# Kernel tuning notes

Hardware: AMD Instinct MI355X
Metric: run time of the kernel (lower is better)

The kernel has to match this reference:

```python
import jax, jax.numpy as jnp
import numpy as np

B, S, M, E, H = 2, 2048, 2048, 1024, 16
D = E // H
LN_EPS = 1e-5


def setup_inputs() -> dict:
    key = jax.random.key(0)
    ks = jax.random.split(key, 14)
    w = lambda k: jax.random.normal(k, (E, E), dtype=jnp.float32) * 0.02
    return {
        "query": jax.random.normal(ks[0], (B, S, E), dtype=jnp.float32),
        "keys": jax.random.normal(ks[1], (B, M, E), dtype=jnp.float32),
        "values": jax.random.normal(ks[2], (B, M, E), dtype=jnp.float32),
        "Wq": w(ks[3]), "bq": jnp.zeros((E,), jnp.float32),
        "Wk": w(ks[4]), "bk": jnp.zeros((E,), jnp.float32),
        "Wv": w(ks[5]), "bv": jnp.zeros((E,), jnp.float32),
        "Wo": w(ks[6]), "bo": jnp.zeros((E,), jnp.float32),
        "gamma": jnp.ones((E,), jnp.float32),
        "beta": jnp.zeros((E,), jnp.float32),
    }


def reference(query, keys, values, Wq, bq, Wk, bk, Wv, bv, Wo, bo, gamma, beta):
    b, s, e = query.shape
    m = keys.shape[1]
    # projections (torch Linear: x @ W.T + b), split heads -> [b, H, len, D]
    Q = (jnp.einsum('bse,fe->bsf', query, Wq) + bq).reshape(b, s, H, D).transpose(0, 2, 1, 3)
    K = (jnp.einsum('bme,fe->bmf', keys, Wk) + bk).reshape(b, m, H, D).transpose(0, 2, 1, 3)
    V = (jnp.einsum('bme,fe->bmf', values, Wv) + bv).reshape(b, m, H, D).transpose(0, 2, 1, 3)
    scores = jnp.einsum('bhsd,bhmd->bhsm', Q, K) / np.sqrt(D).astype(np.float32)
    attn = jax.nn.softmax(scores, axis=-1)  # [b,H,s,m]; dropout is eval no-op
    attended = jnp.einsum('bhsm,bhmd->bhsd', attn, V)
    attended = attended.transpose(0, 2, 1, 3).reshape(b, s, e)
    y = jnp.einsum('bse,fe->bsf', attended, Wo) + bo + query
    mu = jnp.mean(y, axis=-1, keepdims=True)
    var = jnp.mean(jnp.square(y - mu), axis=-1, keepdims=True)
    out = (y - mu) * jax.lax.rsqrt(var + LN_EPS) * gamma + beta
    avg_attention = attn.mean(axis=1)  # [b,s,m]
    return out, avg_attention
```

## Files before the change

kernel.cpp:

```cpp
#include <hip/hip_runtime.h>
#include <hip/hip_bf16.h>

typedef unsigned short u16;
typedef unsigned int   u32;
typedef __attribute__((ext_vector_type(2)))  float fx2;
typedef __attribute__((ext_vector_type(4)))  float fx4;
typedef __attribute__((ext_vector_type(16))) float f32x16;
typedef __attribute__((ext_vector_type(4)))  u16   usx4;
typedef __attribute__((ext_vector_type(8)))  u16   usx8;
typedef __attribute__((ext_vector_type(8)))  __bf16 bf16x8;
typedef __attribute__((ext_vector_type(2)))  int   i32x2;
typedef __attribute__((ext_vector_type(2)))  u32   u32x2;
typedef __attribute__((ext_vector_type(4)))  u32   u32x4;

#define DEVI static __device__ __forceinline__

constexpr int Bb = 2, Ss = 2048, Mm = 2048, Ee = 1024, Hh = 16, Dd = 64;
#define QSCALE 0.18033688011112042f

DEVI u16 f2bf(float f) {
  u32 u = __builtin_bit_cast(u32, f);
  u32 r = (u + 0x7fffu + ((u >> 16) & 1u)) >> 16;
  return (u16)r;
}
DEVI float bf2f(u16 v) {
  u32 u = ((u32)v) << 16;
  return __builtin_bit_cast(float, u);
}
DEVI bf16x8 as_bf(usx8 v) { return __builtin_bit_cast(bf16x8, v); }

DEVI void gld16(const u16* g, u16* l) {
  __builtin_amdgcn_global_load_lds((const __attribute__((address_space(1))) void*)g,
                                   (__attribute__((address_space(3))) void*)l, 16, 0, 0);
}

#if __has_builtin(__builtin_amdgcn_exp2f)
DEVI float xexp2(float x) { return __builtin_amdgcn_exp2f(x); }
#else
DEVI float xexp2(float x) { return exp2f(x); }
#endif

DEVI u32 cvtpk(float lo, float hi) {
  u32 r;
  asm("v_cvt_pk_bf16_f32 %0, %1, %2" : "=v"(r) : "v"(lo), "v"(hi));
  return r;
}
DEVI bf16x8 pa_from(u32 w0, u32 w1, u32 w2, u32 w3) {
  union { u32 u[4]; usx8 v; } t;
  t.u[0] = w0; t.u[1] = w1; t.u[2] = w2; t.u[3] = w3;
  return as_bf(t.v);
}

__global__ __launch_bounds__(256)
void cast_all(const float* __restrict__ q, const float* __restrict__ k,
              const float* __restrict__ v,
              const float* __restrict__ wq, const float* __restrict__ wk,
              const float* __restrict__ wv, const float* __restrict__ wo,
              u16* __restrict__ qc, u16* __restrict__ kc, u16* __restrict__ vc,
              u16* __restrict__ wqc, u16* __restrict__ wkc,
              u16* __restrict__ wvc, u16* __restrict__ woc)
{
  const int y = blockIdx.y;
  const float* s; u16* d; size_t n;
  const size_t NI = (size_t)Bb * Ss * Ee;
  const size_t NW = (size_t)Ee * Ee;
  switch (y) {
    case 0: s = q;  d = qc;  n = NI; break;
    case 1: s = k;  d = kc;  n = NI; break;
    case 2: s = v;  d = vc;  n = NI; break;
    case 3: s = wq; d = wqc; n = NW; break;
    case 4: s = wk; d = wkc; n = NW; break;
    case 5: s = wv; d = wvc; n = NW; break;
    default: s = wo; d = woc; n = NW; break;
  }
  const size_t stride = (size_t)gridDim.x * 256 * 8;
  for (size_t i = ((size_t)blockIdx.x * 256 + threadIdx.x) * 8; i < n; i += stride) {
    fx4 a = *(const fx4*)(s + i);
    fx4 b = *(const fx4*)(s + i + 4);
    u32x4 o;
    o[0] = cvtpk(a[0], a[1]); o[1] = cvtpk(a[2], a[3]);
    o[2] = cvtpk(b[0], b[1]); o[3] = cvtpk(b[2], b[3]);
    *(u32x4*)(d + i) = o;
  }
}

__global__ __launch_bounds__(256, 2)
void gemm_qkv(const u16* __restrict__ qc, const u16* __restrict__ kc,
              const u16* __restrict__ vc,
              const u16* __restrict__ wqc, const u16* __restrict__ wkc,
              const u16* __restrict__ wvc,
              const float* __restrict__ bq, const float* __restrict__ bk,
              const float* __restrict__ bv,
              u16* __restrict__ Qbf, u16* __restrict__ Kbf, u16* __restrict__ Vt)
{
  __shared__ u16 As[2][128][64];
  __shared__ u16 Bs[2][64][64];
  const int tid = threadIdx.x;
  const int w = tid >> 6, l = tid & 63, g = l >> 4, ln = l & 15;
  const int wr = w >> 1, wc = w & 1;

  const int lid = blockIdx.x;
  const int wg = (lid & 7) * 192 + (lid >> 3);
  const int z = wg >> 9;
  const int rem = wg & 511;
  const int row0 = (rem >> 4) * 128;
  const int col0 = (rem & 15) * 64;

  const u16* A = (z == 0) ? qc : (z == 1) ? kc : vc;
  const u16* W = (z == 0) ? wqc : (z == 1) ? wkc : wvc;
  const float* bias = (z == 0) ? bq : (z == 1) ? bk : bv;

  const int colu = (((l & 7) ^ (l >> 3)) << 3);
  auto stage = [&](int buf, int kt) {
#pragma unroll
    for (int j = 0; j < 4; j++) {
      const int c = j * 4 + w;
      const int row = c * 8 + (l >> 3);
      gld16(A + (size_t)(row0 + row) * 1024 + kt * 64 + colu,
            &As[buf][0][0] + c * 512 + l * 8);
    }
#pragma unroll
    for (int j = 0; j < 2; j++) {
      const int c = j * 4 + w;
      const int row = c * 8 + (l >> 3);
      gld16(W + (size_t)(col0 + row) * 1024 + kt * 64 + colu,
            &Bs[buf][0][0] + c * 512 + l * 8);
    }
  };

  fx4 acc[4][2];
#pragma unroll
  for (int i = 0; i < 4; i++)
#pragma unroll
    for (int j = 0; j < 2; j++) acc[i][j] = fx4{0.f, 0.f, 0.f, 0.f};

  stage(0, 0);
  __syncthreads();

  const int swA = (ln & 7) << 3;
  const int NK = 1024 / 64;
  for (int kt = 0; kt < NK; kt++) {
    const int buf = kt & 1;
    if (kt + 1 < NK) stage(buf ^ 1, kt + 1);
#pragma unroll
    for (int ks = 0; ks < 2; ks++) {
      bf16x8 af[4], bfr[2];
      const int cb = (ks * 32 + g * 8) ^ swA;
#pragma unroll
      for (int mi = 0; mi < 4; mi++)
        af[mi] = as_bf(*(const usx8*)&As[buf][wr * 64 + mi * 16 + ln][cb]);
#pragma unroll
      for (int nj = 0; nj < 2; nj++)
        bfr[nj] = as_bf(*(const usx8*)&Bs[buf][wc * 32 + nj * 16 + ln][cb]);
      __builtin_amdgcn_s_setprio(1);
#pragma unroll
      for (int mi = 0; mi < 4; mi++)
#pragma unroll
        for (int nj = 0; nj < 2; nj++)
          acc[mi][nj] = __builtin_amdgcn_mfma_f32_16x16x32_bf16(af[mi], bfr[nj], acc[mi][nj], 0, 0, 0);
      __builtin_amdgcn_s_setprio(0);
    }
    __syncthreads();
  }

#pragma unroll
  for (int mi = 0; mi < 4; mi++) {
#pragma unroll
    for (int nj = 0; nj < 2; nj++) {
      const int j = col0 + wc * 32 + nj * 16 + ln;
      const float bj = bias[j];
      if (z == 2) {
        const int i0 = row0 + wr * 64 + mi * 16 + g * 4;
        const int b2 = i0 >> 11, m2 = i0 & 2047;
        const int h2 = j >> 6,  d2 = j & 63;
        u32x2 pk;
        pk[0] = cvtpk(acc[mi][nj][0] + bj, acc[mi][nj][1] + bj);
        pk[1] = cvtpk(acc[mi][nj][2] + bj, acc[mi][nj][3] + bj);
        *(u32x2*)&Vt[(((size_t)b2 * Hh + h2) * 64 + d2) * (size_t)Mm + m2] = pk;
      } else {
        u16* outp = (z == 0) ? Qbf : Kbf;
        const float sc = (z == 0) ? QSCALE : 1.0f;
#pragma unroll
        for (int r = 0; r < 4; r++) {
          const int i = row0 + wr * 64 + mi * 16 + g * 4 + r;
          outp[(size_t)i * 1024 + j] = f2bf((acc[mi][nj][r] + bj) * sc);
        }
      }
    }
  }
}

__global__ __launch_bounds__(256, 2)
void gemm_out(const u16* __restrict__ Ab, const u16* __restrict__ W,
              const float* __restrict__ bias, const u16* __restrict__ resid,
              u16* __restrict__ outb)
{
  __shared__ u16 As[2][128][64];
  __shared__ u16 Bs[2][64][64];
  const int tid = threadIdx.x;
  const int w = tid >> 6, l = tid & 63, g = l >> 4, ln = l & 15;
  const int wr = w >> 1, wc = w & 1;

  const int lid = blockIdx.x;
  const int wg = (lid & 7) * 64 + (lid >> 3);
  const int row0 = (wg >> 4) * 128;
  const int col0 = (wg & 15) * 64;

  const int colu = (((l & 7) ^ (l >> 3)) << 3);
  auto stage = [&](int buf, int kt) {
#pragma unroll
    for (int j = 0; j < 4; j++) {
      const int c = j * 4 + w;
      const int row = c * 8 + (l >> 3);
      gld16(Ab + (size_t)(row0 + row) * 1024 + kt * 64 + colu,
            &As[buf][0][0] + c * 512 + l * 8);
    }
#pragma unroll
    for (int j = 0; j < 2; j++) {
      const int c = j * 4 + w;
      const int row = c * 8 + (l >> 3);
      gld16(W + (size_t)(col0 + row) * 1024 + kt * 64 + colu,
            &Bs[buf][0][0] + c * 512 + l * 8);
    }
  };

  fx4 acc[4][2];
#pragma unroll
  for (int i = 0; i < 4; i++)
#pragma unroll
    for (int j = 0; j < 2; j++) acc[i][j] = fx4{0.f, 0.f, 0.f, 0.f};

  stage(0, 0);
  __syncthreads();

  const int swA = (ln & 7) << 3;
  const int NK = 1024 / 64;
  for (int kt = 0; kt < NK; kt++) {
    const int buf = kt & 1;
    if (kt + 1 < NK) stage(buf ^ 1, kt + 1);
#pragma unroll
    for (int ks = 0; ks < 2; ks++) {
      bf16x8 af[4], bfr[2];
      const int cb = (ks * 32 + g * 8) ^ swA;
#pragma unroll
      for (int mi = 0; mi < 4; mi++)
        af[mi] = as_bf(*(const usx8*)&As[buf][wr * 64 + mi * 16 + ln][cb]);
#pragma unroll
      for (int nj = 0; nj < 2; nj++)
        bfr[nj] = as_bf(*(const usx8*)&Bs[buf][wc * 32 + nj * 16 + ln][cb]);
      __builtin_amdgcn_s_setprio(1);
#pragma unroll
      for (int mi = 0; mi < 4; mi++)
#pragma unroll
        for (int nj = 0; nj < 2; nj++)
          acc[mi][nj] = __builtin_amdgcn_mfma_f32_16x16x32_bf16(af[mi], bfr[nj], acc[mi][nj], 0, 0, 0);
      __builtin_amdgcn_s_setprio(0);
    }
    __syncthreads();
  }

#pragma unroll
  for (int mi = 0; mi < 4; mi++) {
#pragma unroll
    for (int nj = 0; nj < 2; nj++) {
      const int j = col0 + wc * 32 + nj * 16 + ln;
      const float bj = bias[j];
#pragma unroll
      for (int r = 0; r < 4; r++) {
        const int i = row0 + wr * 64 + mi * 16 + g * 4 + r;
        const float v = acc[mi][nj][r] + bj + bf2f(resid[(size_t)i * 1024 + j]);
        outb[(size_t)i * 1024 + j] = f2bf(v);
      }
    }
  }
}

__global__ __launch_bounds__(256, 2)
void flash_fwd(const u16* __restrict__ Qb, const u16* __restrict__ Kb,
               const u16* __restrict__ Vt, u16* __restrict__ attended,
               float* __restrict__ stats)
{
  __shared__ u16 Ks[2][128][64];
  __shared__ u16 Vs[2][64][128];
  const int tid = threadIdx.x;
  const int w = tid >> 6, l = tid & 63;
  const int ln32 = l & 31, hi = l >> 5;
  const int st = blockIdx.x, h = blockIdx.y, b = blockIdx.z;
  const int s0 = st * 128 + w * 32;

  const u16* Kbase = Kb + (size_t)b * Mm * 1024 + h * 64;
  const u16* Vbase = Vt + ((size_t)(b * Hh + h) * 64) * (size_t)Mm;

  const int colu_k = (((l & 7) ^ (l >> 3)) << 3);
  auto stage = [&](int buf, int mt) {
    const int mb = mt * 128;
#pragma unroll
    for (int j = 0; j < 4; j++) {
      const int c = j * 4 + w;
      const int krow = c * 8 + (l >> 3);
      gld16(Kbase + (size_t)(mb + krow) * 1024 + colu_k,
            &Ks[buf][0][0] + c * 512 + l * 8);
      const int vrow = c * 4 + (l >> 4);
      const int colv = (((l & 15) ^ (vrow & 15)) << 3);
      gld16(Vbase + (size_t)vrow * (size_t)Mm + mb + colv,
            &Vs[buf][0][0] + c * 512 + l * 8);
    }
  };

  bf16x8 qa[4];
#pragma unroll
  for (int dstep = 0; dstep < 4; dstep++)
    qa[dstep] = as_bf(*(const usx8*)(Qb + (size_t)(b * Ss + s0 + ln32) * Ee
                                     + h * 64 + dstep * 16 + hi * 8));

  f32x16 acc[2];
#pragma unroll
  for (int i = 0; i < 16; i++) { acc[0][i] = 0.f; acc[1][i] = 0.f; }
  float lsum = 0.f;

  stage(0, 0);
  __syncthreads();

  const int NT = Mm / 128;
  for (int mt = 0; mt < NT; mt++) {
    const int buf = mt & 1;
    if (mt + 1 < NT) stage(buf ^ 1, mt + 1);

    f32x16 sc[4];
#pragma unroll
    for (int mtile = 0; mtile < 4; mtile++) {
      const int row = mtile * 32 + ln32;
      const int sw = (row & 7) << 3;
      f32x16 c;
#pragma unroll
      for (int i = 0; i < 16; i++) c[i] = 0.f;
#pragma unroll
      for (int dstep = 0; dstep < 4; dstep++) {
        bf16x8 kf = as_bf(*(const usx8*)&Ks[buf][row][(dstep * 16 + hi * 8) ^ sw]);
        c = __builtin_amdgcn_mfma_f32_32x32x16_bf16(kf, qa[dstep], c, 0, 0, 0);
      }
      sc[mtile] = c;
    }

#pragma unroll
    for (int mtile = 0; mtile < 4; mtile++) {
      float p[16];
#pragma unroll
      for (int r = 0; r < 16; r++) p[r] = xexp2(sc[mtile][r]);
      float t0 = (p[0] + p[1]) + (p[2] + p[3]);
      float t1 = (p[4] + p[5]) + (p[6] + p[7]);
      float t2 = (p[8] + p[9]) + (p[10] + p[11]);
      float t3 = (p[12] + p[13]) + (p[14] + p[15]);
      lsum += (t0 + t1) + (t2 + t3);

      u32 cp[8];
#pragma unroll
      for (int i = 0; i < 8; i++) cp[i] = cvtpk(p[2 * i], p[2 * i + 1]);
      i32x2 sA = __builtin_amdgcn_permlane32_swap((int)cp[0], (int)cp[2], false, false);
      i32x2 sB = __builtin_amdgcn_permlane32_swap((int)cp[1], (int)cp[3], false, false);
      bf16x8 pa0 = pa_from((u32)sA.x, (u32)sB.x, (u32)sA.y, (u32)sB.y);
      i32x2 sC = __builtin_amdgcn_permlane32_swap((int)cp[4], (int)cp[6], false, false);
      i32x2 sD = __builtin_amdgcn_permlane32_swap((int)cp[5], (int)cp[7], false, false);
      bf16x8 pa1 = pa_from((u32)sC.x, (u32)sD.x, (u32)sC.y, (u32)sD.y);

#pragma unroll
      for (int dtile = 0; dtile < 2; dtile++) {
        const int vrow = dtile * 32 + ln32;
        const int vsw = (vrow & 15) << 3;
        bf16x8 vb0 = as_bf(*(const usx8*)&Vs[buf][vrow][(mtile * 32 + hi * 8) ^ vsw]);
        bf16x8 vb1 = as_bf(*(const usx8*)&Vs[buf][vrow][(mtile * 32 + 16 + hi * 8) ^ vsw]);
        acc[dtile] = __builtin_amdgcn_mfma_f32_32x32x16_bf16(pa0, vb0, acc[dtile], 0, 0, 0);
        acc[dtile] = __builtin_amdgcn_mfma_f32_32x32x16_bf16(pa1, vb1, acc[dtile], 0, 0, 0);
      }
    }
    __syncthreads();
  }

  lsum += __shfl_xor(lsum, 32);
  const float inv = 1.0f / lsum;
  if (l < 32)
    stats[(size_t)(b * Hh + h) * Ss + s0 + l] = inv;
#pragma unroll
  for (int r = 0; r < 16; r++) {
    const int srow = (r & 3) + 8 * (r >> 2) + 4 * hi;
    const float invr = __shfl(inv, srow);
    const int s_abs = s0 + srow;
#pragma unroll
    for (int dtile = 0; dtile < 2; dtile++)
      attended[(size_t)(b * Ss + s_abs) * Ee + h * 64 + dtile * 32 + ln32] =
          f2bf(acc[dtile][r] * invr);
  }
}

__global__ __launch_bounds__(256)
void avg_attn(const u16* __restrict__ Qb, const u16* __restrict__ Kb,
              const float* __restrict__ stats, float* __restrict__ avg_out)
{
  __shared__ u16 Ks[3][64][64];
  const int tid = threadIdx.x;
  const int w = tid >> 6, l = tid & 63;
  const int ln32 = l & 31, hi = l >> 5;
  const int mtile0 = blockIdx.x, stile = blockIdx.y, b = blockIdx.z;
  const int m0 = mtile0 * 64;
  const int s0 = stile * 128 + w * 32;
  const int s_lane = s0 + ln32;

  const u16* Kbase = Kb + (size_t)(b * Mm + m0) * 1024;
  const u16* Qrow  = Qb + (size_t)(b * Ss + s_lane) * Ee;
  const float* strow = stats + (size_t)b * Hh * Ss + s_lane;

  const int colu = (((l & 7) ^ (l >> 3)) << 3);
  auto stage = [&](int slot, int h) {
#pragma unroll
    for (int j = 0; j < 2; j++) {
      const int c = j * 4 + w;
      const int row = c * 8 + (l >> 3);
      gld16(Kbase + (size_t)row * 1024 + h * 64 + colu,
            &Ks[slot][0][0] + c * 512 + l * 8);
    }
  };

  f32x16 acc[2];
#pragma unroll
  for (int i = 0; i < 16; i++) { acc[0][i] = 0.f; acc[1][i] = 0.f; }

  stage(0, 0);
  stage(1, 1);
  asm volatile("s_waitcnt vmcnt(2)" ::: "memory");
  __builtin_amdgcn_s_barrier();

  for (int h = 0; h < Hh; h++) {
    const int slot = h % 3;

    bf16x8 qa[4];
#pragma unroll
    for (int d = 0; d < 4; d++)
      qa[d] = as_bf(*(const usx8*)(Qrow + h * 64 + d * 16 + hi * 8));
    const float invh = strow[(size_t)h * Ss];

    if (h + 2 < Hh) stage((h + 2) % 3, h + 2);

#pragma unroll
    for (int mtile = 0; mtile < 2; mtile++) {
      const int row = mtile * 32 + ln32;
      const int sw = (row & 7) << 3;
      f32x16 c;
#pragma unroll
      for (int i = 0; i < 16; i++) c[i] = 0.f;
      __builtin_amdgcn_s_setprio(1);
#pragma unroll
      for (int dstep = 0; dstep < 4; dstep++) {
        bf16x8 kf = as_bf(*(const usx8*)&Ks[slot][row][(dstep * 16 + hi * 8) ^ sw]);
        c = __builtin_amdgcn_mfma_f32_32x32x16_bf16(kf, qa[dstep], c, 0, 0, 0);
      }
      __builtin_amdgcn_s_setprio(0);
#pragma unroll
      for (int r = 0; r < 16; r++)
        acc[mtile][r] += xexp2(c[r]) * invh;
    }

    if (h + 2 < Hh) {
      asm volatile("s_waitcnt vmcnt(2)" ::: "memory");
    } else {
      asm volatile("s_waitcnt vmcnt(0)" ::: "memory");
    }
    __builtin_amdgcn_s_barrier();
  }

  float* orow = avg_out + ((size_t)(b * Ss + s_lane)) * Mm + m0;
#pragma unroll
  for (int mtile = 0; mtile < 2; mtile++)
#pragma unroll
    for (int rq = 0; rq < 4; rq++) {
      fx4 o;
#pragma unroll
      for (int j = 0; j < 4; j++) o[j] = acc[mtile][rq * 4 + j] * (1.0f / 16.0f);
      *(fx4*)(orow + mtile * 32 + rq * 8 + 4 * hi) = o;
    }
}

__global__ __launch_bounds__(256)
void ln_kernel(const u16* __restrict__ yb, const float* __restrict__ gamma,
               const float* __restrict__ beta, float* __restrict__ out)
{
  const int row = blockIdx.x, tid = threadIdx.x;
  const int w = tid >> 6, l = tid & 63;
  usx4 v4 = *(const usx4*)(yb + (size_t)row * 1024 + tid * 4);
  float v[4];
#pragma unroll
  for (int j = 0; j < 4; j++) v[j] = bf2f(v4[j]);
  float s = v[0] + v[1] + v[2] + v[3];
  float s2 = v[0] * v[0] + v[1] * v[1] + v[2] * v[2] + v[3] * v[3];
#pragma unroll
  for (int off = 32; off >= 1; off >>= 1) {
    s += __shfl_xor(s, off);
    s2 += __shfl_xor(s2, off);
  }
  __shared__ float rs[4], rq[4];
  if (l == 0) { rs[w] = s; rq[w] = s2; }
  __syncthreads();
  s = (rs[0] + rs[1]) + (rs[2] + rs[3]);
  s2 = (rq[0] + rq[1]) + (rq[2] + rq[3]);
  const float mu = s * (1.0f / 1024.0f);
  const float var = s2 * (1.0f / 1024.0f) - mu * mu;
  const float rstd = rsqrtf(var + 1e-5f);
  fx4 gm = *(const fx4*)(gamma + tid * 4);
  fx4 bt = *(const fx4*)(beta + tid * 4);
  fx4 o;
#pragma unroll
  for (int j = 0; j < 4; j++) o[j] = (v[j] - mu) * rstd * gm[j] + bt[j];
  *(fx4*)(out + (size_t)row * 1024 + tid * 4) = o;
}

extern "C" void kernel_launch(void* const* d_in, const int* in_sizes, int n_in,
                              void* d_out, int out_size, void* d_ws, size_t ws_size,
                              hipStream_t stream)
{
  const float* query = (const float*)d_in[0];
  const float* keys  = (const float*)d_in[1];
  const float* values = (const float*)d_in[2];
  const float* Wq = (const float*)d_in[3];  const float* bq = (const float*)d_in[4];
  const float* Wk = (const float*)d_in[5];  const float* bk = (const float*)d_in[6];
  const float* Wv = (const float*)d_in[7];  const float* bv = (const float*)d_in[8];
  const float* Wo = (const float*)d_in[9];  const float* bo = (const float*)d_in[10];
  const float* gamma = (const float*)d_in[11];
  const float* beta  = (const float*)d_in[12];

  float* out = (float*)d_out;
  float* avg_out = out + (size_t)Bb * Ss * Ee;

  const size_t MB = 1024 * 1024;
  char* ws = (char*)d_ws;
  u16*   Qbf    = (u16*)(ws);
  u16*   Kbf    = (u16*)(ws + 8  * MB);
  u16*   Vt     = (u16*)(ws + 16 * MB);
  u16*   qc     = (u16*)(ws + 24 * MB);
  u16*   kc     = (u16*)(ws + 32 * MB);
  u16*   vc     = (u16*)(ws + 40 * MB);
  u16*   wqc    = (u16*)(ws + 48 * MB);
  u16*   wkc    = (u16*)(ws + 50 * MB);
  u16*   wvc    = (u16*)(ws + 52 * MB);
  u16*   woc    = (u16*)(ws + 54 * MB);
  float* stats  = (float*)(ws + 56 * MB);
  u16*   att_bf = (u16*)(ws + 32 * MB);
  u16*   ybuf   = (u16*)(ws + 40 * MB);

  cast_all<<<dim3(512, 7), 256, 0, stream>>>(query, keys, values, Wq, Wk, Wv, Wo,
                                             qc, kc, vc, wqc, wkc, wvc, woc);

  gemm_qkv<<<dim3(1536), 256, 0, stream>>>(qc, kc, vc, wqc, wkc, wvc,
                                           bq, bk, bv, Qbf, Kbf, Vt);

  flash_fwd<<<dim3(Ss / 128, Hh, Bb), 256, 0, stream>>>(Qbf, Kbf, Vt, att_bf, stats);
  avg_attn<<<dim3(Mm / 64, Ss / 128, Bb), 256, 0, stream>>>(Qbf, Kbf, stats, avg_out);

  gemm_out<<<dim3(512), 256, 0, stream>>>(att_bf, woc, bo, qc, ybuf);
  ln_kernel<<<dim3(Bb * Ss), 256, 0, stream>>>(ybuf, gamma, beta, out);
}
```

Baseline: 161.4 us.

## Triple-buffer flash attention K/V tiles with 64-row tiles and manual vmcnt waits

Switches the attention kernel from double-buffered 128-key tiles to triple-buffered 64-key tiles. Loads are issued two tiles ahead, and the full __syncthreads is replaced by an explicit vmcnt wait plus s_barrier, so global loads stay in flight across iterations. Score and PV work are now interleaved per 32-row subtile, dropping the sc[4] register array, and s_setprio is raised around MFMA sections. Shared memory use drops, which may help occupancy, but the kernel now runs twice as many barriers. The vmcnt counts are hand-tuned and depend on how the compiler orders the loads.

```diff
diff --git a/kernel.cpp b/kernel.cpp
--- a/kernel.cpp
+++ b/kernel.cpp
@@ -280,8 +280,8 @@
                const u16* __restrict__ Vt, u16* __restrict__ attended,
                float* __restrict__ stats)
 {
-  __shared__ u16 Ks[2][128][64];
-  __shared__ u16 Vs[2][64][128];
+  __shared__ u16 Ks[3][64][64];
+  __shared__ u16 Vs[3][64][64];
   const int tid = threadIdx.x;
   const int w = tid >> 6, l = tid & 63;
   const int ln32 = l & 31, hi = l >> 5;
@@ -291,19 +291,22 @@
   const u16* Kbase = Kb + (size_t)b * Mm * 1024 + h * 64;
   const u16* Vbase = Vt + ((size_t)(b * Hh + h) * 64) * (size_t)Mm;
 
-  const int colu_k = (((l & 7) ^ (l >> 3)) << 3);
-  auto stage = [&](int buf, int mt) {
-    const int mb = mt * 128;
-#pragma unroll
-    for (int j = 0; j < 4; j++) {
-      const int c = j * 4 + w;
-      const int krow = c * 8 + (l >> 3);
-      gld16(Kbase + (size_t)(mb + krow) * 1024 + colu_k,
-            &Ks[buf][0][0] + c * 512 + l * 8);
-      const int vrow = c * 4 + (l >> 4);
-      const int colv = (((l & 15) ^ (vrow & 15)) << 3);
-      gld16(Vbase + (size_t)vrow * (size_t)Mm + mb + colv,
-            &Vs[buf][0][0] + c * 512 + l * 8);
+  const int colu = (((l & 7) ^ (l >> 3)) << 3);
+  auto stage = [&](int slot, int mt) {
+    const int mb = mt * 64;
+#pragma unroll
+    for (int j = 0; j < 2; j++) {
+      const int c = j * 4 + w;
+      const int row = c * 8 + (l >> 3);
+      gld16(Kbase + (size_t)(mb + row) * 1024 + colu,
+            &Ks[slot][0][0] + c * 512 + l * 8);
+    }
+#pragma unroll
+    for (int j = 0; j < 2; j++) {
+      const int c = j * 4 + w;
+      const int vrow = c * 8 + (l >> 3);
+      gld16(Vbase + (size_t)vrow * (size_t)Mm + mb + colu,
+            &Vs[slot][0][0] + c * 512 + l * 8);
     }
   };
 
@@ -319,34 +322,33 @@
   float lsum = 0.f;
 
   stage(0, 0);
-  __syncthreads();
-
-  const int NT = Mm / 128;
+  stage(1, 1);
+  asm volatile("s_waitcnt vmcnt(4)" ::: "memory");
+  __builtin_amdgcn_s_barrier();
+
+  const int NT = Mm / 64;
   for (int mt = 0; mt < NT; mt++) {
-    const int buf = mt & 1;
-    if (mt + 1 < NT) stage(buf ^ 1, mt + 1);
-
-    f32x16 sc[4];
-#pragma unroll
-    for (int mtile = 0; mtile < 4; mtile++) {
+    const int slot = mt % 3;
+    if (mt + 2 < NT) stage((mt + 2) % 3, mt + 2);
+
+#pragma unroll
+    for (int mtile = 0; mtile < 2; mtile++) {
       const int row = mtile * 32 + ln32;
       const int sw = (row & 7) << 3;
       f32x16 c;
 #pragma unroll
       for (int i = 0; i < 16; i++) c[i] = 0.f;
+      __builtin_amdgcn_s_setprio(1);
 #pragma unroll
       for (int dstep = 0; dstep < 4; dstep++) {
-        bf16x8 kf = as_bf(*(const usx8*)&Ks[buf][row][(dstep * 16 + hi * 8) ^ sw]);
+        bf16x8 kf = as_bf(*(const usx8*)&Ks[slot][row][(dstep * 16 + hi * 8) ^ sw]);
         c = __builtin_amdgcn_mfma_f32_32x32x16_bf16(kf, qa[dstep], c, 0, 0, 0);
       }
-      sc[mtile] = c;
-    }
-
-#pragma unroll
-    for (int mtile = 0; mtile < 4; mtile++) {
+      __builtin_amdgcn_s_setprio(0);
+
       float p[16];
 #pragma unroll
-      for (int r = 0; r < 16; r++) p[r] = xexp2(sc[mtile][r]);
+      for (int r = 0; r < 16; r++) p[r] = xexp2(c[r]);
       float t0 = (p[0] + p[1]) + (p[2] + p[3]);
       float t1 = (p[4] + p[5]) + (p[6] + p[7]);
       float t2 = (p[8] + p[9]) + (p[10] + p[11]);
@@ -363,17 +365,25 @@
       i32x2 sD = __builtin_amdgcn_permlane32_swap((int)cp[5], (int)cp[7], false, false);
       bf16x8 pa1 = pa_from((u32)sC.x, (u32)sD.x, (u32)sC.y, (u32)sD.y);
 
+      __builtin_amdgcn_s_setprio(1);
 #pragma unroll
       for (int dtile = 0; dtile < 2; dtile++) {
         const int vrow = dtile * 32 + ln32;
-        const int vsw = (vrow & 15) << 3;
-        bf16x8 vb0 = as_bf(*(const usx8*)&Vs[buf][vrow][(mtile * 32 + hi * 8) ^ vsw]);
-        bf16x8 vb1 = as_bf(*(const usx8*)&Vs[buf][vrow][(mtile * 32 + 16 + hi * 8) ^ vsw]);
+        const int vsw = (vrow & 7) << 3;
+        bf16x8 vb0 = as_bf(*(const usx8*)&Vs[slot][vrow][(mtile * 32 + hi * 8) ^ vsw]);
+        bf16x8 vb1 = as_bf(*(const usx8*)&Vs[slot][vrow][(mtile * 32 + 16 + hi * 8) ^ vsw]);
         acc[dtile] = __builtin_amdgcn_mfma_f32_32x32x16_bf16(pa0, vb0, acc[dtile], 0, 0, 0);
         acc[dtile] = __builtin_amdgcn_mfma_f32_32x32x16_bf16(pa1, vb1, acc[dtile], 0, 0, 0);
       }
-    }
-    __syncthreads();
+      __builtin_amdgcn_s_setprio(0);
+    }
+
+    if (mt + 2 < NT) {
+      asm volatile("s_waitcnt vmcnt(4)" ::: "memory");
+    } else {
+      asm volatile("s_waitcnt vmcnt(0)" ::: "memory");
+    }
+    __builtin_amdgcn_s_barrier();
   }
 
   lsum += __shfl_xor(lsum, 32);
```

New measurement: 167.7 us. +3.9%, slower.
